# Optimization experiments

Hardware: AMD Instinct MI355X
Metric: run time of the kernel (lower is better)

The kernel has to match this reference:

```python
import jax, jax.numpy as jnp
import numpy as np

START_TAG = 7
STOP_TAG = 8
NEG = -10000.0  # matches torch.full((1,K), -10000.) in the original


def setup_inputs() -> dict:
    key = jax.random.key(0)
    k1, k2, k3, k4 = jax.random.split(key, 4)
    B, T, K = 1024, 2048, 9  # K = output_dim + 2 (START/STOP hardcoded as 7/8)
    feats = jax.random.normal(k1, (B, T, K), dtype=jnp.float32)
    tags = jax.random.randint(k2, (B, T), 0, 7)            # valid labels 0..6
    lengths = jax.random.randint(k3, (B,), 1, T + 1)        # per-sentence lengths >= 1
    transitions = jax.random.normal(k4, (K, K), dtype=jnp.float32)
    transitions = transitions.at[START_TAG, :].set(NEG)     # never transition into START
    transitions = transitions.at[:, STOP_TAG].set(NEG)      # never transition out of STOP
    return {"feats": feats, "transitions": transitions, "tags": tags, "lengths": lengths}


def _crf_nll(feats, transitions, tags, lengths):
    # feats: [B,T,K] emissions, transitions[j,i] = score of i -> j
    B, T, K = feats.shape

    def fwd_one(feat, length):
        # CRF forward algorithm (log partition), vectorized over tags,
        # lax.scan over time; masked past `length` to emulate feats[:x_len].
        alpha0 = jnp.full((K,), NEG, feat.dtype).at[START_TAG].set(0.0)

        def step(alpha, inp):
            t, f = inp
            # alpha_new[j] = logsumexp_i(alpha[i] + transitions[j,i]) + feat[t,j]
            new = jax.nn.logsumexp(alpha[None, :] + transitions, axis=1) + f
            return jnp.where(t < length, new, alpha), None

        alpha, _ = jax.lax.scan(step, alpha0, (jnp.arange(T), feat))
        return jax.nn.logsumexp(alpha + transitions[STOP_TAG])

    fwd_scores = jax.vmap(fwd_one)(feats, lengths)  # [B]

    def gold_one(feat, tg, length):
        # _score_sentence: sum_t trans[tags[t], tags[t-1]] + feat[t, tags[t]]
        prev = jnp.concatenate([jnp.array([START_TAG], tg.dtype), tg[:-1]])
        step_scores = transitions[tg, prev] + jnp.take_along_axis(feat, tg[:, None], axis=1)[:, 0]
        mask = jnp.arange(tg.shape[0]) < length
        last = tg[length - 1]
        return jnp.sum(jnp.where(mask, step_scores, 0.0)) + transitions[STOP_TAG, last]

    gold_scores = jax.vmap(gold_one)(feats, tags, lengths)  # [B]

    # neg_log_likelihood accumulates (forward - gold) per sentence, then / n
    return jnp.mean(fwd_scores - gold_scores)


def reference(feats, transitions, tags, lengths):
    return _crf_nll(feats, transitions, tags, lengths)
```

## Files before the change

kernel.cpp:

```cpp
#include <hip/hip_runtime.h>


#define START_TAG 7
#define STOP_TAG  8
#define KDIM      9
#define NS        7
#define CHUNKS    32
#define NEGINF    (-1e30f)

__device__ __forceinline__ float rfl(float x) {
    return __int_as_float(__builtin_amdgcn_readfirstlane(__float_as_int(x)));
}

__global__ __launch_bounds__(256) void crf_fused_kernel(
    const float* __restrict__ feats,
    const float* __restrict__ trans,
    const int*   __restrict__ tags,
    const int*   __restrict__ lengths,
    float* __restrict__ out,
    int B, int T, int L)
{
    __shared__ float s_trans[81];
    __shared__ float s_E[49];
    __shared__ float s_M[CHUNKS * 64];
    __shared__ float s_gold[4];

    const int tid = threadIdx.x;
    const int b   = blockIdx.x;

    if (tid < 81) s_trans[tid] = trans[tid];
    if (tid >= 128 && tid < 128 + 49) {
        int k = tid - 128;
        s_E[k] = __expf(trans[(k / 7) * 9 + (k % 7)]);
    }
    __syncthreads();

    const int    len   = lengths[b];
    const int*   tg    = tags  + (size_t)b * T;
    const float* fbase = feats + (size_t)b * T * KDIM;

    {
        int per = T >> 8;
        int t0  = tid * per;
        float g = 0.f;
        if (t0 < len) {
            int te   = min(t0 + per, len);
            int prev = (t0 == 0) ? START_TAG : tg[t0 - 1];
            for (int t = t0; t < te; ++t) {
                int cur = tg[t];
                g += s_trans[cur * 9 + prev] + fbase[(size_t)t * KDIM + cur];
                prev = cur;
            }
            if (len - 1 < t0 + per) g += s_trans[STOP_TAG * 9 + tg[len - 1]];
        }
        #pragma unroll
        for (int off = 32; off > 0; off >>= 1) g += __shfl_xor(g, off, 64);
        if ((tid & 63) == 0) s_gold[tid >> 6] = g;
    }

    {
        const int lane8 = tid & 7;
        const int c     = tid >> 3;
        const int t0    = c * L;
        const int tstart = max(t0, 1);
        const int tend   = min(t0 + L, len);

        if (lane8 < NS) {
            const int col = lane8;
            float* Mw = s_M + c * 64;
            if (tstart < tend) {
                float E[49];
                #pragma unroll
                for (int k = 0; k < 49; ++k) E[k] = rfl(s_E[k]);

                float p[NS];
                #pragma unroll
                for (int j = 0; j < NS; ++j) p[j] = (j == col) ? 1.f : 0.f;
                float s = 0.f;

                const float* fp = fbase + (size_t)tstart * KDIM;
                int steps = tend - tstart;

                #define CRF_STEP() do {                                         \
                    float4 fA = *(const float4*)fp;                             \
                    float4 fB = *(const float4*)(fp + 4);                       \
                    fp += KDIM;                                                 \
                    float f[NS] = {fA.x, fA.y, fA.z, fA.w, fB.x, fB.y, fB.z};   \
                    float q[NS];                                                \
                    _Pragma("unroll")                                           \
                    for (int j = 0; j < NS; ++j) {                              \
                        float acc = E[j * 7] * p[0];                            \
                        _Pragma("unroll")                                       \
                        for (int i = 1; i < NS; ++i)                            \
                            acc = fmaf(E[j * 7 + i], p[i], acc);                \
                        q[j] = acc * __expf(f[j]);                              \
                    }                                                           \
                    _Pragma("unroll")                                           \
                    for (int j = 0; j < NS; ++j) p[j] = q[j];                   \
                } while (0)

                #define CRF_RENORM() do {                                       \
                    float m = p[0];                                             \
                    _Pragma("unroll")                                           \
                    for (int j = 1; j < NS; ++j) m = fmaxf(m, p[j]);            \
                    float rm = __builtin_amdgcn_rcpf(m);                        \
                    _Pragma("unroll")                                           \
                    for (int j = 0; j < NS; ++j) p[j] *= rm;                    \
                    s += __logf(m);                                             \
                } while (0)

                while (steps >= 4) {
                    CRF_STEP(); CRF_STEP(); CRF_STEP(); CRF_STEP();
                    CRF_RENORM();
                    steps -= 4;
                }
                if (steps > 0) {
                    while (steps-- > 0) { CRF_STEP(); }
                    CRF_RENORM();
                }

                #pragma unroll
                for (int j = 0; j < NS; ++j)
                    Mw[j * 8 + col] = __logf(p[j]) + s;
            } else {
                #pragma unroll
                for (int j = 0; j < NS; ++j)
                    Mw[j * 8 + col] = (j == col) ? 0.f : NEGINF;
            }
        }
    }
    __syncthreads();

    if (tid < 8) {
        const int lane = tid;
        const bool isrow = (lane < NS);
        const int row = isrow ? lane : 0;

        float a, S;
        {
            float a0 = isrow ? (s_trans[lane * 9 + START_TAG] + fbase[lane]) : NEGINF;
            float m = a0;
            #pragma unroll
            for (int off = 4; off > 0; off >>= 1) m = fmaxf(m, __shfl_xor(m, off, 8));
            a = a0 - m;
            S = m;
        }

        const int nc = (len + L - 1) / L;
        for (int c = 0; c < nc; ++c) {
            const float* Mr = s_M + c * 64 + row * 8;
            float tv[NS];
            float tm = NEGINF;
            #pragma unroll
            for (int i = 0; i < NS; ++i) {
                float ai = __shfl(a, i, 8);
                tv[i] = Mr[i] + ai;
                tm = fmaxf(tm, tv[i]);
            }
            float sum = 0.f;
            #pragma unroll
            for (int i = 0; i < NS; ++i) sum += __expf(tv[i] - tm);
            float na = tm + __logf(sum);
            float m2 = na;
            #pragma unroll
            for (int off = 4; off > 0; off >>= 1) m2 = fmaxf(m2, __shfl_xor(m2, off, 8));
            a = na - m2;
            S += m2;
        }

        float term = isrow ? (a + s_trans[STOP_TAG * 9 + lane]) : NEGINF;
        float tm2 = term;
        #pragma unroll
        for (int off = 4; off > 0; off >>= 1) tm2 = fmaxf(tm2, __shfl_xor(tm2, off, 8));
        float e = isrow ? __expf(term - tm2) : 0.f;
        #pragma unroll
        for (int off = 4; off > 0; off >>= 1) e += __shfl_xor(e, off, 8);

        if (lane == 0) {
            float fwd = S + tm2 + __logf(e);
            float g = s_gold[0] + s_gold[1] + s_gold[2] + s_gold[3];
            atomicAdd(out, (fwd - g) * (1.0f / (float)B));
        }
    }
}

__global__ void init_out_kernel(float* out) {
    if (threadIdx.x == 0) out[0] = 0.f;
}

extern "C" void kernel_launch(void* const* d_in, const int* in_sizes, int n_in,
                              void* d_out, int out_size, void* d_ws, size_t ws_size,
                              hipStream_t stream) {
    const float* feats   = (const float*)d_in[0];
    const float* trans   = (const float*)d_in[1];
    const int*   tags    = (const int*)d_in[2];
    const int*   lengths = (const int*)d_in[3];

    int B = in_sizes[3];
    int T = in_sizes[2] / B;
    int L = (T + CHUNKS - 1) / CHUNKS;

    init_out_kernel<<<1, 64, 0, stream>>>((float*)d_out);
    crf_fused_kernel<<<B, 256, 0, stream>>>(
        feats, trans, tags, lengths, (float*)d_out, B, T, L);
}
```

Before: 167.6 us.

## Distribute exp of emissions across lanes and software-pipeline feature loads

In the chunked forward recurrence, each lane now loads and exponentiates only its own emission column, and the values are broadcast to the other lanes with ds_bpermute. Before, every lane loaded two float4s and computed seven exps per step. Emission loads are prefetched one 4-step group ahead, and the merge loop prefetches the next chunk's matrix row. The gold-score loop is unrolled with clamped indices so it has no data-dependent branch. The cost is seven cross-lane permutes per step on the critical dependency chain, which could add latency compared with the redundant exps.

```diff
diff --git a/kernel.cpp b/kernel.cpp
--- a/kernel.cpp
+++ b/kernel.cpp
@@ -29,7 +29,7 @@
     const int b   = blockIdx.x;
 
     if (tid < 81) s_trans[tid] = trans[tid];
-    if (tid >= 128 && tid < 128 + 49) {
+    if (tid >= 128 && tid < 177) {
         int k = tid - 128;
         s_E[k] = __expf(trans[(k / 7) * 9 + (k % 7)]);
     }
@@ -40,18 +40,34 @@
     const float* fbase = feats + (size_t)b * T * KDIM;
 
     {
-        int per = T >> 8;
+        int per = (T >> 8) > 0 ? (T >> 8) : 1;
         int t0  = tid * per;
         float g = 0.f;
         if (t0 < len) {
             int te   = min(t0 + per, len);
             int prev = (t0 == 0) ? START_TAG : tg[t0 - 1];
-            for (int t = t0; t < te; ++t) {
-                int cur = tg[t];
-                g += s_trans[cur * 9 + prev] + fbase[(size_t)t * KDIM + cur];
-                prev = cur;
+            if (per == 8) {
+                #pragma unroll
+                for (int k = 0; k < 8; ++k) {
+                    int t   = t0 + k;
+                    int tc  = min(t, te - 1);
+                    int cur = tg[tc];
+                    float v = s_trans[cur * 9 + prev] + fbase[(size_t)tc * KDIM + cur];
+                    g += (t < te) ? v : 0.f;
+                    prev = cur;
+                }
+            } else {
+                for (int k = 0; k < per; ++k) {
+                    int t   = t0 + k;
+                    int tc  = min(t, te - 1);
+                    int cur = tg[tc];
+                    float v = s_trans[cur * 9 + prev] + fbase[(size_t)tc * KDIM + cur];
+                    g += (t < te) ? v : 0.f;
+                    prev = cur;
+                }
             }
-            if (len - 1 < t0 + per) g += s_trans[STOP_TAG * 9 + tg[len - 1]];
+            if (len - 1 >= t0 && len - 1 < t0 + per)
+                g += s_trans[STOP_TAG * 9 + tg[len - 1]];
         }
         #pragma unroll
         for (int off = 32; off > 0; off >>= 1) g += __shfl_xor(g, off, 64);
@@ -59,33 +75,32 @@
     }
 
     {
-        const int lane8 = tid & 7;
-        const int c     = tid >> 3;
-        const int t0    = c * L;
+        const int lane8  = tid & 7;
+        const int c      = tid >> 3;
+        const int t0     = c * L;
         const int tstart = max(t0, 1);
         const int tend   = min(t0 + L, len);
 
         if (lane8 < NS) {
-            const int col = lane8;
             float* Mw = s_M + c * 64;
             if (tstart < tend) {
                 float E[49];
                 #pragma unroll
                 for (int k = 0; k < 49; ++k) E[k] = rfl(s_E[k]);
 
+                int baddr[NS];
+                #pragma unroll
+                for (int j = 0; j < NS; ++j) baddr[j] = (((tid & 56) | j) << 2);
+
                 float p[NS];
                 #pragma unroll
-                for (int j = 0; j < NS; ++j) p[j] = (j == col) ? 1.f : 0.f;
+                for (int j = 0; j < NS; ++j) p[j] = (j == lane8) ? 1.f : 0.f;
                 float s = 0.f;
-
-                const float* fp = fbase + (size_t)tstart * KDIM;
-                int steps = tend - tstart;
-
-                #define CRF_STEP() do {                                         \
-                    float4 fA = *(const float4*)fp;                             \
-                    float4 fB = *(const float4*)(fp + 4);                       \
-                    fp += KDIM;                                                 \
-                    float f[NS] = {fA.x, fA.y, fA.z, fA.w, fB.x, fB.y, fB.z};   \
+                int rem = tend - tstart;
+
+                const float* fp = fbase + (size_t)tstart * KDIM + lane8;
+
+                #define CRF_STEP(XF) do {                                       \
                     float q[NS];                                                \
                     _Pragma("unroll")                                           \
                     for (int j = 0; j < NS; ++j) {                              \
@@ -93,10 +108,16 @@
                         _Pragma("unroll")                                       \
                         for (int i = 1; i < NS; ++i)                            \
                             acc = fmaf(E[j * 7 + i], p[i], acc);                \
-                        q[j] = acc * __expf(f[j]);                              \
+                        q[j] = acc;                                             \
                     }                                                           \
-                    _Pragma("unroll")                                           \
-                    for (int j = 0; j < NS; ++j) p[j] = q[j];                   \
+                    float myef = __expf(XF);                                    \
+                    _Pragma("unroll")                                           \
+                    for (int j = 0; j < NS; ++j) {                              \
+                        float efj = __int_as_float(                             \
+                            __builtin_amdgcn_ds_bpermute(                       \
+                                baddr[j], __float_as_int(myef)));               \
+                        p[j] = q[j] * efj;                                      \
+                    }                                                           \
                 } while (0)
 
                 #define CRF_RENORM() do {                                       \
@@ -109,32 +130,52 @@
                     s += __logf(m);                                             \
                 } while (0)
 
-                while (steps >= 4) {
-                    CRF_STEP(); CRF_STEP(); CRF_STEP(); CRF_STEP();
+                int o1 = KDIM * min(1, rem - 1);
+                int o2 = KDIM * min(2, rem - 1);
+                int o3 = KDIM * min(3, rem - 1);
+                float x0 = fp[0], x1 = fp[o1], x2 = fp[o2], x3 = fp[o3];
+                fp += 4 * KDIM;
+
+                while (rem >= 8) {
+                    float y0 = fp[0], y1 = fp[KDIM], y2 = fp[2 * KDIM], y3 = fp[3 * KDIM];
+                    fp += 4 * KDIM;
+                    CRF_STEP(x0); CRF_STEP(x1); CRF_STEP(x2); CRF_STEP(x3);
                     CRF_RENORM();
-                    steps -= 4;
-                }
-                if (steps > 0) {
-                    while (steps-- > 0) { CRF_STEP(); }
+                    x0 = y0; x1 = y1; x2 = y2; x3 = y3;
+                    rem -= 4;
+                }
+                if (rem > 4) {
+                    int e1 = KDIM * min(1, rem - 5);
+                    int e2 = KDIM * min(2, rem - 5);
+                    float y0 = fp[0], y1 = fp[e1], y2 = fp[e2];
+                    CRF_STEP(x0); CRF_STEP(x1); CRF_STEP(x2); CRF_STEP(x3);
                     CRF_RENORM();
-                }
+                    x0 = y0; x1 = y1; x2 = y2;
+                    rem -= 4;
+                }
+                CRF_STEP(x0);
+                if (rem > 1) CRF_STEP(x1);
+                if (rem > 2) CRF_STEP(x2);
+                if (rem > 3) CRF_STEP(x3);
 
                 #pragma unroll
                 for (int j = 0; j < NS; ++j)
-                    Mw[j * 8 + col] = __logf(p[j]) + s;
+                    Mw[j * 8 + lane8] = __logf(p[j]) + s;
+                #undef CRF_STEP
+                #undef CRF_RENORM
             } else {
                 #pragma unroll
                 for (int j = 0; j < NS; ++j)
-                    Mw[j * 8 + col] = (j == col) ? 0.f : NEGINF;
+                    Mw[j * 8 + lane8] = (j == lane8) ? 0.f : NEGINF;
             }
         }
     }
     __syncthreads();
 
     if (tid < 8) {
-        const int lane = tid;
+        const int  lane  = tid;
         const bool isrow = (lane < NS);
-        const int row = isrow ? lane : 0;
+        const int  row   = isrow ? lane : 0;
 
         float a, S;
         {
@@ -146,26 +187,31 @@
             S = m;
         }
 
-        const int nc = (len + L - 1) / L;
+        const int nc = min(CHUNKS, (len + L - 1) / L);
+        const float* Mr0 = s_M + row * 8;
+        float4 mA = *(const float4*)(Mr0);
+        float4 mB = *(const float4*)(Mr0 + 4);
         for (int c = 0; c < nc; ++c) {
-            const float* Mr = s_M + c * 64 + row * 8;
-            float tv[NS];
+            int cn = min(c + 1, CHUNKS - 1);
+            float4 nA = *(const float4*)(Mr0 + cn * 64);
+            float4 nB = *(const float4*)(Mr0 + cn * 64 + 4);
+            float tv[NS] = { mA.x, mA.y, mA.z, mA.w, mB.x, mB.y, mB.z };
             float tm = NEGINF;
             #pragma unroll
             for (int i = 0; i < NS; ++i) {
-                float ai = __shfl(a, i, 8);
-                tv[i] = Mr[i] + ai;
+                tv[i] += __shfl(a, i, 8);
                 tm = fmaxf(tm, tv[i]);
             }
             float sum = 0.f;
             #pragma unroll
             for (int i = 0; i < NS; ++i) sum += __expf(tv[i] - tm);
-            float na = tm + __logf(sum);
+            float na = isrow ? (tm + __logf(sum)) : NEGINF;
             float m2 = na;
             #pragma unroll
             for (int off = 4; off > 0; off >>= 1) m2 = fmaxf(m2, __shfl_xor(m2, off, 8));
             a = na - m2;
             S += m2;
+            mA = nA; mB = nB;
         }
 
         float term = isrow ? (a + s_trans[STOP_TAG * 9 + lane]) : NEGINF;
```

New measurement: 157.0 us. 6.4% less time.
